# Performance work log

Hardware: AMD Instinct MI355X
Metric: run time of the kernel (lower is better)

## Reference

```python
import jax, jax.numpy as jnp
import numpy as np

HID = 512
IN = 256
B = 64
T = 1024
ALPHA0 = 10.0 / 100.0  # dt / tau


def setup_inputs() -> dict:
    key = jax.random.key(0)
    k1, k2, k3, k4, k5 = jax.random.split(key, 5)
    x = jax.random.normal(k1, (B, T, IN), dtype=jnp.float32)
    init_state = jnp.zeros((B, HID), dtype=jnp.float32)
    W_in = jax.random.normal(k2, (IN, HID), dtype=jnp.float32) / np.sqrt(IN)
    b_in = jnp.zeros((HID,), dtype=jnp.float32)
    W_hid = jax.random.normal(k3, (HID, HID), dtype=jnp.float32) / np.sqrt(HID)
    b_hid = jnp.zeros((HID,), dtype=jnp.float32)
    alpha = jnp.full((HID,), ALPHA0, dtype=jnp.float32)
    return {"x": x, "init_state": init_state, "W_in": W_in, "b_in": b_in,
            "W_hid": W_hid, "b_hid": b_hid, "alpha": alpha}


def reference(x, init_state, W_in, b_in, W_hid, b_hid, alpha):
    # Precompute input projection for all timesteps (same math, batched GEMM)
    v_in = jnp.einsum('bti,ih->bth', x, W_in) + b_in  # (B, T, HID)

    def step(carry, v_in_t):
        fr_t, v_t = carry
        v_hid_t = fr_t @ W_hid + b_hid            # (B, HID)
        v_t = (1.0 - alpha) * v_t + alpha * (v_hid_t + v_in_t)
        fr_t = jax.nn.relu(v_t)
        return (fr_t, v_t), fr_t

    v0 = init_state
    fr0 = jax.nn.relu(v0)
    # scan over time axis
    _, frs = jax.lax.scan(step, (fr0, v0), jnp.swapaxes(v_in, 0, 1))
    return jnp.swapaxes(frs, 0, 1)  # (B, T, HID)
```

## Files before the change

### kernel.cpp

```cpp
#include <hip/hip_runtime.h>

#define HID 512
#define TSTEPS 1024

typedef short bf16x8 __attribute__((ext_vector_type(8)));
typedef float fx4 __attribute__((ext_vector_type(4)));
typedef unsigned ux2 __attribute__((ext_vector_type(2)));

__device__ __forceinline__ short f2bf(float f) {
  unsigned u = __builtin_bit_cast(unsigned, f);
  u = (u + 0x7fffu + ((u >> 16) & 1u)) >> 16;
  return (short)u;
}

__global__ __launch_bounds__(256) void vin_gemm(
    const float* __restrict__ x, const float* __restrict__ W_in,
    const float* __restrict__ b_in, const float* __restrict__ b_hid,
    float* __restrict__ out)
{
  __shared__ __align__(16) char smA[128 * 32 * 2];
  __shared__ __align__(16) char smB[128 * 32 * 2];
  const int tid = threadIdx.x;
  const int wave = tid >> 6, lane = tid & 63;
  const int lg = lane >> 4, lr = lane & 15;
  const int wm = wave >> 1, wn = wave & 1;
  const int r0 = blockIdx.x * 128, c0 = blockIdx.y * 128;

  fx4 acc[4][4] = {};

  const int arow = tid >> 3, aseg = tid & 7;
  const int bk = tid >> 3, bq = tid & 7;

  for (int k0 = 0; k0 < 256; k0 += 32) {
    #pragma unroll
    for (int q = 0; q < 4; ++q) {
      int row = arow + q * 32;
      fx4 fv = *(const fx4*)(x + (size_t)(r0 + row) * 256 + k0 + aseg * 4);
      ux2 p;
      p[0] = (unsigned)(unsigned short)f2bf(fv[0]) | ((unsigned)(unsigned short)f2bf(fv[1]) << 16);
      p[1] = (unsigned)(unsigned short)f2bf(fv[2]) | ((unsigned)(unsigned short)f2bf(fv[3]) << 16);
      int addr = (row * 64 + aseg * 8) ^ ((row & 7) << 4);
      *(ux2*)(smA + addr) = p;
    }
    #pragma unroll
    for (int q = 0; q < 4; ++q) {
      fx4 fv = *(const fx4*)(W_in + (size_t)(k0 + bk) * HID + c0 + q * 32 + bq * 4);
      #pragma unroll
      for (int e = 0; e < 4; ++e) {
        int col = q * 32 + bq * 4 + e;
        int addr = (col * 64 + bk * 2) ^ ((col & 7) << 4);
        *(short*)(smB + addr) = f2bf(fv[e]);
      }
    }
    __syncthreads();
    bf16x8 af[4];
    #pragma unroll
    for (int mt = 0; mt < 4; ++mt) {
      int row = wm * 64 + mt * 16 + lr;
      af[mt] = *(const bf16x8*)(smA + ((row * 64 + lg * 16) ^ ((row & 7) << 4)));
    }
    #pragma unroll
    for (int nt = 0; nt < 4; ++nt) {
      int col = wn * 64 + nt * 16 + lr;
      bf16x8 bf = *(const bf16x8*)(smB + ((col * 64 + lg * 16) ^ ((col & 7) << 4)));
      #pragma unroll
      for (int mt = 0; mt < 4; ++mt)
        acc[mt][nt] = __builtin_amdgcn_mfma_f32_16x16x32_bf16(af[mt], bf, acc[mt][nt], 0, 0, 0);
    }
    __syncthreads();
  }
  float bi[4];
  #pragma unroll
  for (int nt = 0; nt < 4; ++nt) {
    int c = c0 + wn * 64 + nt * 16 + lr;
    bi[nt] = b_in[c] + b_hid[c];
  }
  #pragma unroll
  for (int mt = 0; mt < 4; ++mt)
    #pragma unroll
    for (int nt = 0; nt < 4; ++nt)
      #pragma unroll
      for (int jj = 0; jj < 4; ++jj) {
        int grow = r0 + wm * 64 + mt * 16 + lg * 4 + jj;
        int gcol = c0 + wn * 64 + nt * 16 + lr;
        out[(size_t)grow * HID + gcol] = acc[mt][nt][jj] + bi[nt];
      }
}

#define FR0_OFF (128 * 1024)

__global__ __launch_bounds__(512, 2) void rnn_scan(
    float* base,
    const float* __restrict__ init_state,
    const float* __restrict__ W_hid,
    const float* __restrict__ alpha)
{
  extern __shared__ __align__(16) char smem[];
  const int tid = threadIdx.x;
  const int wave = tid >> 6, lane = tid & 63;
  const int lg = lane >> 4, lr = lane & 15;
  const int bwg = blockIdx.x;
  const int cb = wave * 64;

  bf16x8 wreg[3][16];
  #pragma unroll
  for (int nt = 0; nt < 4; ++nt) {
    const int col = cb + nt * 16 + lr;
    #pragma unroll
    for (int kk = 0; kk < 16; ++kk) {
      const int k0 = kk * 32 + lg * 8;
      bf16x8 w;
      #pragma unroll
      for (int j = 0; j < 8; ++j)
        w[j] = f2bf(W_hid[(size_t)(k0 + j) * HID + col]);
      if (nt < 3) {
        wreg[nt][kk] = w;
      } else {
        const int cw = wave * 16 + lr;
        int addr = (cw * 1024 + kk * 64 + lg * 16) ^ ((cw & 7) << 4);
        *(bf16x8*)(smem + addr) = w;
      }
    }
  }

  float al[4], v[4][4];
  #pragma unroll
  for (int nt = 0; nt < 4; ++nt) al[nt] = alpha[cb + nt * 16 + lr];
  #pragma unroll
  for (int nt = 0; nt < 4; ++nt)
    #pragma unroll
    for (int jj = 0; jj < 4; ++jj)
      v[nt][jj] = init_state[(size_t)(bwg * 16 + lg * 4 + jj) * HID + cb + nt * 16 + lr];

  #pragma unroll
  for (int nt = 0; nt < 4; ++nt)
    #pragma unroll
    for (int jj = 0; jj < 4; ++jj) {
      int row = lg * 4 + jj;
      int addr = (FR0_OFF + row * 1024 + (cb + nt * 16 + lr) * 2) ^ ((row & 7) << 4);
      *(short*)(smem + addr) = f2bf(fmaxf(v[nt][jj], 0.f));
    }

  int off[4];
  #pragma unroll
  for (int jj = 0; jj < 4; ++jj)
    off[jj] = (lg * 4 + jj) * TSTEPS * HID + cb + lr;
  float* bb = base + (size_t)bwg * 16 * TSTEPS * HID;

  float vld[4][4];
  #pragma unroll
  for (int nt = 0; nt < 4; ++nt)
    #pragma unroll
    for (int jj = 0; jj < 4; ++jj)
      vld[nt][jj] = bb[off[jj] + nt * 16];

  __syncthreads();

  const int aswz = (lr & 7) << 4;
  const int abase0 = lr * 1024 + lg * 16;
  const int cw = wave * 16 + lr;
  const int wbase = cw * 1024 + lg * 16;
  const int wswz = (cw & 7) << 4;

  for (int t = 0; t < TSTEPS; ++t) {
    const int rb = FR0_OFF + ((t & 1) << 14);
    const int wb = FR0_OFF + (((t + 1) & 1) << 14);

    fx4 acc[4];
    #pragma unroll
    for (int nt = 0; nt < 4; ++nt)
      #pragma unroll
      for (int jj = 0; jj < 4; ++jj)
        acc[nt][jj] = vld[nt][jj];

    #pragma unroll
    for (int kk = 0; kk < 16; ++kk) {
      bf16x8 a  = *(const bf16x8*)(smem + ((rb + abase0 + kk * 64) ^ aswz));
      bf16x8 b3 = *(const bf16x8*)(smem + ((wbase + kk * 64) ^ wswz));
      acc[0] = __builtin_amdgcn_mfma_f32_16x16x32_bf16(a, wreg[0][kk], acc[0], 0, 0, 0);
      acc[1] = __builtin_amdgcn_mfma_f32_16x16x32_bf16(a, wreg[1][kk], acc[1], 0, 0, 0);
      acc[2] = __builtin_amdgcn_mfma_f32_16x16x32_bf16(a, wreg[2][kk], acc[2], 0, 0, 0);
      acc[3] = __builtin_amdgcn_mfma_f32_16x16x32_bf16(a, b3,          acc[3], 0, 0, 0);
    }

    #pragma unroll
    for (int nt = 0; nt < 4; ++nt)
      #pragma unroll
      for (int jj = 0; jj < 4; ++jj) {
        float nv = v[nt][jj] + al[nt] * (acc[nt][jj] - v[nt][jj]);
        v[nt][jj] = nv;
        float fr = fmaxf(nv, 0.f);
        bb[t * HID + off[jj] + nt * 16] = fr;
        int row = lg * 4 + jj;
        int addr = (wb + row * 1024 + (cb + nt * 16 + lr) * 2) ^ ((row & 7) << 4);
        *(short*)(smem + addr) = f2bf(fr);
      }

    if (t + 1 < TSTEPS) {
      #pragma unroll
      for (int nt = 0; nt < 4; ++nt)
        #pragma unroll
        for (int jj = 0; jj < 4; ++jj)
          vld[nt][jj] = bb[(t + 1) * HID + off[jj] + nt * 16];
    }

    __syncthreads();
  }
}

extern "C" void kernel_launch(void* const* d_in, const int* in_sizes, int n_in,
                              void* d_out, int out_size, void* d_ws, size_t ws_size,
                              hipStream_t stream) {
  const float* x     = (const float*)d_in[0];
  const float* inist = (const float*)d_in[1];
  const float* W_in  = (const float*)d_in[2];
  const float* b_in  = (const float*)d_in[3];
  const float* W_hid = (const float*)d_in[4];
  const float* b_hid = (const float*)d_in[5];
  const float* alph  = (const float*)d_in[6];
  float* out = (float*)d_out;
  (void)in_sizes; (void)n_in; (void)out_size; (void)d_ws; (void)ws_size;

  vin_gemm<<<dim3(512, 4), dim3(256), 0, stream>>>(x, W_in, b_in, b_hid, out);

  (void)hipFuncSetAttribute(reinterpret_cast<const void*>(rnn_scan),
                            hipFuncAttributeMaxDynamicSharedMemorySize, 160 * 1024);
  rnn_scan<<<dim3(4), dim3(512), 160 * 1024, stream>>>(out, inist, W_hid, alph);
}
```

Before: 4.940 ms.

## Stream one W_hid column tile from global/L2 each step to free registers

Moves one of the three register-resident W_hid column tiles into a pre-packed bf16 workspace built by a new pack_w kernel. The scan kernel now streams that tile from global memory (L2-resident) in chunks during each step's MFMA loop. It also changes the fr smem swizzle to a lane-group based XOR and removes the vld->acc copy by loading v_in directly into the accumulators. The intent is to cut register pressure and spills and to reduce LDS bank conflicts, at the cost of extra global loads on the serial critical path every timestep.

Result: faster. 4.078 ms (-17.4%).

```diff
diff --git a/kernel.cpp b/kernel.cpp
--- a/kernel.cpp
+++ b/kernel.cpp
@@ -87,13 +87,30 @@
       }
 }
 
+__global__ __launch_bounds__(512) void pack_w(const float* __restrict__ W_hid,
+                                              short* __restrict__ ws)
+{
+  const int tid = threadIdx.x;
+  const int wave = tid >> 6, lane = tid & 63;
+  const int lg = lane >> 4, lr = lane & 15;
+  const int col = wave * 64 + 32 + lr;
+  for (int kk = 0; kk < 16; ++kk) {
+    bf16x8 w;
+    #pragma unroll
+    for (int j = 0; j < 8; ++j)
+      w[j] = f2bf(W_hid[(size_t)(kk * 32 + lg * 8 + j) * HID + col]);
+    *(bf16x8*)(ws + ((size_t)((wave * 16 + kk) * 64 + lane)) * 8) = w;
+  }
+}
+
 #define FR0_OFF (128 * 1024)
 
 __global__ __launch_bounds__(512, 2) void rnn_scan(
     float* base,
     const float* __restrict__ init_state,
     const float* __restrict__ W_hid,
-    const float* __restrict__ alpha)
+    const float* __restrict__ alpha,
+    const short* __restrict__ wsf)
 {
   extern __shared__ __align__(16) char smem[];
   const int tid = threadIdx.x;
@@ -102,9 +119,10 @@
   const int bwg = blockIdx.x;
   const int cb = wave * 64;
 
-  bf16x8 wreg[3][16];
+  bf16x8 wreg[2][16];
   #pragma unroll
   for (int nt = 0; nt < 4; ++nt) {
+    if (nt == 2) continue;
     const int col = cb + nt * 16 + lr;
     #pragma unroll
     for (int kk = 0; kk < 16; ++kk) {
@@ -113,7 +131,7 @@
       #pragma unroll
       for (int j = 0; j < 8; ++j)
         w[j] = f2bf(W_hid[(size_t)(k0 + j) * HID + col]);
-      if (nt < 3) {
+      if (nt < 2) {
         wreg[nt][kk] = w;
       } else {
         const int cw = wave * 16 + lr;
@@ -137,7 +155,7 @@
     #pragma unroll
     for (int jj = 0; jj < 4; ++jj) {
       int row = lg * 4 + jj;
-      int addr = (FR0_OFF + row * 1024 + (cb + nt * 16 + lr) * 2) ^ ((row & 7) << 4);
+      int addr = (FR0_OFF + row * 1024 + (cb + nt * 16 + lr) * 2) ^ (lg << 5);
       *(short*)(smem + addr) = f2bf(fmaxf(v[nt][jj], 0.f));
     }
 
@@ -147,39 +165,49 @@
     off[jj] = (lg * 4 + jj) * TSTEPS * HID + cb + lr;
   float* bb = base + (size_t)bwg * 16 * TSTEPS * HID;
 
-  float vld[4][4];
+  fx4 acc[4];
   #pragma unroll
   for (int nt = 0; nt < 4; ++nt)
     #pragma unroll
     for (int jj = 0; jj < 4; ++jj)
-      vld[nt][jj] = bb[off[jj] + nt * 16];
+      acc[nt][jj] = bb[off[jj] + nt * 16];
+
+  const bf16x8* wsp = (const bf16x8*)(wsf + ((size_t)(wave * 16) * 64 + lane) * 8);
+  bf16x8 wst[16];
+  wst[0] = wsp[0];   wst[1] = wsp[64];  wst[2] = wsp[128]; wst[3] = wsp[192];
 
   __syncthreads();
 
-  const int aswz = (lr & 7) << 4;
+  const int aswz = (lr >> 2) << 5;
   const int abase0 = lr * 1024 + lg * 16;
   const int cw = wave * 16 + lr;
   const int wbase = cw * 1024 + lg * 16;
   const int wswz = (cw & 7) << 4;
+  const int frwswz = lg << 5;
 
   for (int t = 0; t < TSTEPS; ++t) {
     const int rb = FR0_OFF + ((t & 1) << 14);
     const int wb = FR0_OFF + (((t + 1) & 1) << 14);
 
-    fx4 acc[4];
-    #pragma unroll
-    for (int nt = 0; nt < 4; ++nt)
-      #pragma unroll
-      for (int jj = 0; jj < 4; ++jj)
-        acc[nt][jj] = vld[nt][jj];
-
     #pragma unroll
     for (int kk = 0; kk < 16; ++kk) {
+      if (kk == 0) {
+        wst[4] = wsp[4 * 64];  wst[5] = wsp[5 * 64];
+        wst[6] = wsp[6 * 64];  wst[7] = wsp[7 * 64];
+      }
+      if (kk == 4) {
+        wst[8]  = wsp[8 * 64];  wst[9]  = wsp[9 * 64];
+        wst[10] = wsp[10 * 64]; wst[11] = wsp[11 * 64];
+      }
+      if (kk == 8) {
+        wst[12] = wsp[12 * 64]; wst[13] = wsp[13 * 64];
+        wst[14] = wsp[14 * 64]; wst[15] = wsp[15 * 64];
+      }
       bf16x8 a  = *(const bf16x8*)(smem + ((rb + abase0 + kk * 64) ^ aswz));
       bf16x8 b3 = *(const bf16x8*)(smem + ((wbase + kk * 64) ^ wswz));
       acc[0] = __builtin_amdgcn_mfma_f32_16x16x32_bf16(a, wreg[0][kk], acc[0], 0, 0, 0);
       acc[1] = __builtin_amdgcn_mfma_f32_16x16x32_bf16(a, wreg[1][kk], acc[1], 0, 0, 0);
-      acc[2] = __builtin_amdgcn_mfma_f32_16x16x32_bf16(a, wreg[2][kk], acc[2], 0, 0, 0);
+      acc[2] = __builtin_amdgcn_mfma_f32_16x16x32_bf16(a, wst[kk],     acc[2], 0, 0, 0);
       acc[3] = __builtin_amdgcn_mfma_f32_16x16x32_bf16(a, b3,          acc[3], 0, 0, 0);
     }
 
@@ -192,7 +220,7 @@
         float fr = fmaxf(nv, 0.f);
         bb[t * HID + off[jj] + nt * 16] = fr;
         int row = lg * 4 + jj;
-        int addr = (wb + row * 1024 + (cb + nt * 16 + lr) * 2) ^ ((row & 7) << 4);
+        int addr = (wb + row * 1024 + (cb + nt * 16 + lr) * 2) ^ frwswz;
         *(short*)(smem + addr) = f2bf(fr);
       }
 
@@ -201,8 +229,9 @@
       for (int nt = 0; nt < 4; ++nt)
         #pragma unroll
         for (int jj = 0; jj < 4; ++jj)
-          vld[nt][jj] = bb[(t + 1) * HID + off[jj] + nt * 16];
-    }
+          acc[nt][jj] = bb[(t + 1) * HID + off[jj] + nt * 16];
+    }
+    wst[0] = wsp[0];   wst[1] = wsp[64];  wst[2] = wsp[128]; wst[3] = wsp[192];
 
     __syncthreads();
   }
@@ -219,11 +248,13 @@
   const float* b_hid = (const float*)d_in[5];
   const float* alph  = (const float*)d_in[6];
   float* out = (float*)d_out;
-  (void)in_sizes; (void)n_in; (void)out_size; (void)d_ws; (void)ws_size;
-
+  (void)in_sizes; (void)n_in; (void)out_size; (void)ws_size;
+
+  pack_w<<<dim3(1), dim3(512), 0, stream>>>(W_hid, (short*)d_ws);
   vin_gemm<<<dim3(512, 4), dim3(256), 0, stream>>>(x, W_in, b_in, b_hid, out);
 
   (void)hipFuncSetAttribute(reinterpret_cast<const void*>(rnn_scan),
                             hipFuncAttributeMaxDynamicSharedMemorySize, 160 * 1024);
-  rnn_scan<<<dim3(4), dim3(512), 160 * 1024, stream>>>(out, inist, W_hid, alph);
-}
+  rnn_scan<<<dim3(4), dim3(512), 160 * 1024, stream>>>(out, inist, W_hid, alph,
+                                                       (const short*)d_ws);
+}
```
